# Kernel tuning notes

Hardware: AMD Instinct MI355X
Metric: run time of the kernel (lower is better)

## Reference

```python
import jax, jax.numpy as jnp
import numpy as np

N_NODES = 50000
N_EDGES = 1600000
CHANNELS = 128
EXPANSION = 50
CUTOFF = 5.0
LOG2 = 0.6931471805599453


def shifted_softplus(x):
    return jax.nn.softplus(x) - LOG2


def gaussian_smearing(r, cutoff=CUTOFF, n=EXPANSION):
    # centers evenly spaced in [0, cutoff]; width set by spacing
    centers = jnp.linspace(0.0, cutoff, n, dtype=r.dtype)
    delta = centers[1] - centers[0]
    coef = 1.0 / (2.0 * delta * delta)
    d = r[:, None] - centers[None, :]          # [E, n]
    return jnp.exp(-coef * d * d)


def setup_inputs() -> dict:
    key = jax.random.key(0)
    ks = jax.random.split(key, 12)
    C, F = CHANNELS, EXPANSION

    def lin(k, fan_in, shape):
        bound = 1.0 / np.sqrt(fan_in)
        return jax.random.uniform(k, shape, jnp.float32, -bound, bound)

    return {
        "features": jax.random.normal(ks[0], (N_NODES, C), jnp.float32),
        "edge_distances": jax.random.uniform(ks[1], (N_EDGES,), jnp.float32) * CUTOFF,
        "W_lin": lin(ks[2], C, (C, C)),
        "Wf1": lin(ks[3], F, (F, C)), "bf1": lin(ks[4], F, (C,)),
        "Wf2": lin(ks[5], C, (C, C)), "bf2": lin(ks[6], C, (C,)),
        "Wm1": lin(ks[7], C, (C, C)), "bm1": lin(ks[8], C, (C,)),
        "Wm2": lin(ks[9], C, (C, C)), "bm2": lin(ks[10], C, (C,)),
        "senders": jax.random.randint(ks[11], (N_EDGES,), 0, N_NODES, jnp.int32),
        "receivers": jax.random.randint(jax.random.fold_in(key, 99), (N_EDGES,), 0, N_NODES, jnp.int32),
    }


def reference(features, edge_distances, W_lin, Wf1, bf1, Wf2, bf2,
              Wm1, bm1, Wm2, bm2, senders, receivers):
    # 1. linear transform of node features (no bias)
    h = features @ W_lin.T                                   # [N, C]
    # 2. learnable radial filter F(r_ij): Gaussian basis -> MLP
    basis = gaussian_smearing(edge_distances)                # [E, F]
    ef = shifted_softplus(basis @ Wf1 + bf1) @ Wf2 + bf2     # [E, C]
    # 3. gather neighbour features, elementwise multiply, scatter-sum
    messages = h[senders] * ef                               # [E, C]
    agg = jax.ops.segment_sum(messages, receivers, num_segments=N_NODES)  # [N, C]
    # 4. output MLP
    return shifted_softplus(agg @ Wm1 + bm1) @ Wm2 + bm2
```

## Files before the change

kernel.cpp:

```cpp
#include <hip/hip_runtime.h>
#include <hip/hip_bf16.h>
#include <math.h>

#define N_NODES 50000
#define N_EDGES 1600000
#define CH 128
#define NF 50
#define NR 8192
#define NB 512
#define BUCKET_NODES 98
#define CAP 3584
#define PASSA_CHUNK 4096
#define NBLK_SCAT 391
#define NBLK_TB   128
#define NBLK_DH   782
#define GATHER_NPB 16
#define NBLK_GATH 3125

constexpr float DELTA  = 5.0f / 49.0f;
constexpr float COEF   = 1.0f / (2.0f * DELTA * DELTA);
constexpr float LOG2_  = 0.6931471805599453f;
constexpr float RSCALE = (float)(NR - 1) / 5.0f;

typedef short  bf16x8 __attribute__((ext_vector_type(8)));
typedef float  f32x4  __attribute__((ext_vector_type(4)));
typedef unsigned short ushort_t;
typedef unsigned long long u64;

__device__ __forceinline__ float ssp(float x) {
    return fmaxf(x, 0.0f) + __logf(1.0f + __expf(-fabsf(x))) - LOG2_;
}
__device__ __forceinline__ ushort_t f2bf(float x) {
    __hip_bfloat16 b = __float2bfloat16(x);
    return *reinterpret_cast<ushort_t*>(&b);
}
__device__ __forceinline__ float bf2f(ushort_t u) {
    return __uint_as_float(((unsigned)u) << 16);
}
__device__ __forceinline__ float4 f4zero() { return make_float4(0.f, 0.f, 0.f, 0.f); }

__global__ __launch_bounds__(256) void k1_prep(const float* __restrict__ Wlin,
                                               const float* __restrict__ Wm1,
                                               const float* __restrict__ Wm2,
                                               const float* __restrict__ Wf1,
                                               const float* __restrict__ Wf2,
                                               ushort_t* __restrict__ wlhi,
                                               ushort_t* __restrict__ wllo,
                                               ushort_t* __restrict__ wm1hi,
                                               ushort_t* __restrict__ wm1lo,
                                               ushort_t* __restrict__ wm2hi,
                                               ushort_t* __restrict__ wm2lo,
                                               ushort_t* __restrict__ wf1t,
                                               ushort_t* __restrict__ wf2hi,
                                               ushort_t* __restrict__ wf2lo,
                                               int* __restrict__ bcnt) {
    const int tid = threadIdx.x;
    if (blockIdx.x == 64) {
        bcnt[tid] = 0;
        bcnt[tid + 256] = 0;
        return;
    }
    int idx = blockIdx.x * 256 + tid;
    int n = idx >> 7, k = idx & 127;
    {   float w = Wlin[(size_t)n * CH + k];
        ushort_t hi = f2bf(w); wlhi[n * CH + k] = hi; wllo[n * CH + k] = f2bf(w - bf2f(hi)); }
    {   float w = Wm1[(size_t)k * CH + n];
        ushort_t hi = f2bf(w); wm1hi[n * CH + k] = hi; wm1lo[n * CH + k] = f2bf(w - bf2f(hi)); }
    {   float w = Wm2[(size_t)k * CH + n];
        ushort_t hi = f2bf(w); wm2hi[n * CH + k] = hi; wm2lo[n * CH + k] = f2bf(w - bf2f(hi)); }
    if (k < 64) wf1t[n * 64 + k] = (k < NF) ? f2bf(Wf1[k * CH + n]) : (ushort_t)0;
    {   float w = Wf2[(size_t)k * CH + n];
        ushort_t hi = f2bf(w); wf2hi[n * CH + k] = hi; wf2lo[n * CH + k] = f2bf(w - bf2f(hi)); }
}

__device__ void scatter_body(char* smem, int blk,
                             const int* __restrict__ recv,
                             const int* __restrict__ send,
                             const float* __restrict__ dist,
                             int* __restrict__ bcnt,
                             u64* __restrict__ brec) {
    int* bcur   = (int*)smem;
    int* bbaseL = bcur + NB;
    const int tid = threadIdx.x;
    for (int i = tid; i < NB; i += 256) bcur[i] = 0;
    __syncthreads();
    const int e0 = blk * PASSA_CHUNK;
#pragma unroll
    for (int i = 0; i < 16; i++) {
        int e = e0 + tid + i * 256;
        if (e < N_EDGES) atomicAdd(&bcur[recv[e] / BUCKET_NODES], 1);
    }
    __syncthreads();
    for (int i = tid; i < NB; i += 256) {
        int c = bcur[i];
        bbaseL[i] = c ? atomicAdd(&bcnt[i], c) : 0;
        bcur[i] = 0;
    }
    __syncthreads();
#pragma unroll
    for (int i = 0; i < 16; i++) {
        int e = e0 + tid + i * 256;
        if (e < N_EDGES) {
            int r = recv[e];
            int b = r / BUCKET_NODES;
            int rank = bbaseL[b] + atomicAdd(&bcur[b], 1);
            if (rank < CAP) {
                float x = fminf(dist[e] * RSCALE, (float)(NR - 1));
                int ti = __float2int_rn(x);
                u64 rec = (u64)(unsigned)(send[e] | (r << 16)) | ((u64)ti << 32);
                brec[(size_t)b * CAP + rank] = rec;
            }
        }
    }
}

__device__ void table_body(char* smem, int blk,
                           const float* __restrict__ bf1,
                           const float* __restrict__ bf2,
                           const ushort_t* __restrict__ wf1t,
                           const ushort_t* __restrict__ wf2hi,
                           const ushort_t* __restrict__ wf2lo,
                           ushort_t* __restrict__ tabn) {
    ushort_t (*basis)[72] = (ushort_t (*)[72])smem;
    ushort_t (*t1s)[136]  = (ushort_t (*)[136])(smem + 64 * 72 * 2);
    const int tid = threadIdx.x;
    const int g0  = blk * 64;

    for (int i = tid; i < 64 * 64; i += 256) {
        int e = i >> 6, k = i & 63;
        float val = 0.f;
        if (k < NF) {
            float r = (float)(g0 + e) * (5.0f / (float)(NR - 1));
            float d = r - (float)k * DELTA;
            val = __expf(-COEF * d * d);
        }
        basis[e][k] = f2bf(val);
    }
    __syncthreads();

    const int lane = tid & 63;
    const int wv   = tid >> 6;
    const int row  = lane & 15;
    const int quad = lane >> 4;
    const int c0   = (2 * wv) * 16 + row;
    const int c1   = c0 + 16;

    f32x4 acc[2][4];
#pragma unroll
    for (int j = 0; j < 2; j++)
#pragma unroll
        for (int rt = 0; rt < 4; rt++) acc[j][rt] = (f32x4){0.f, 0.f, 0.f, 0.f};

#pragma unroll
    for (int kb = 0; kb < 64; kb += 32) {
        bf16x8 B0 = *(const bf16x8*)&wf1t[c0 * 64 + kb + quad * 8];
        bf16x8 B1 = *(const bf16x8*)&wf1t[c1 * 64 + kb + quad * 8];
#pragma unroll
        for (int rt = 0; rt < 4; rt++) {
            bf16x8 A = *(const bf16x8*)&basis[rt * 16 + row][kb + quad * 8];
            acc[0][rt] = __builtin_amdgcn_mfma_f32_16x16x32_bf16(A, B0, acc[0][rt], 0, 0, 0);
            acc[1][rt] = __builtin_amdgcn_mfma_f32_16x16x32_bf16(A, B1, acc[1][rt], 0, 0, 0);
        }
    }
    {
        float b1v[2] = { bf1[c0], bf1[c1] };
#pragma unroll
        for (int j = 0; j < 2; j++) {
            int c = j ? c1 : c0;
#pragma unroll
            for (int rt = 0; rt < 4; rt++)
#pragma unroll
                for (int rg = 0; rg < 4; rg++) {
                    int e = rt * 16 + quad * 4 + rg;
                    t1s[e][c] = f2bf(ssp(acc[j][rt][rg] + b1v[j]));
                }
        }
    }
    __syncthreads();

#pragma unroll
    for (int j = 0; j < 2; j++)
#pragma unroll
        for (int rt = 0; rt < 4; rt++) acc[j][rt] = (f32x4){0.f, 0.f, 0.f, 0.f};

#pragma unroll
    for (int kb = 0; kb < 128; kb += 32) {
        bf16x8 B0h = *(const bf16x8*)&wf2hi[c0 * CH + kb + quad * 8];
        bf16x8 B0l = *(const bf16x8*)&wf2lo[c0 * CH + kb + quad * 8];
        bf16x8 B1h = *(const bf16x8*)&wf2hi[c1 * CH + kb + quad * 8];
        bf16x8 B1l = *(const bf16x8*)&wf2lo[c1 * CH + kb + quad * 8];
#pragma unroll
        for (int rt = 0; rt < 4; rt++) {
            bf16x8 A = *(const bf16x8*)&t1s[rt * 16 + row][kb + quad * 8];
            acc[0][rt] = __builtin_amdgcn_mfma_f32_16x16x32_bf16(A, B0l, acc[0][rt], 0, 0, 0);
            acc[0][rt] = __builtin_amdgcn_mfma_f32_16x16x32_bf16(A, B0h, acc[0][rt], 0, 0, 0);
            acc[1][rt] = __builtin_amdgcn_mfma_f32_16x16x32_bf16(A, B1l, acc[1][rt], 0, 0, 0);
            acc[1][rt] = __builtin_amdgcn_mfma_f32_16x16x32_bf16(A, B1h, acc[1][rt], 0, 0, 0);
        }
    }
    {
        float b2v[2] = { bf2[c0], bf2[c1] };
#pragma unroll
        for (int j = 0; j < 2; j++) {
            int c = j ? c1 : c0;
#pragma unroll
            for (int rt = 0; rt < 4; rt++)
#pragma unroll
                for (int rg = 0; rg < 4; rg++) {
                    int g = g0 + rt * 16 + quad * 4 + rg;
                    tabn[(size_t)g * CH + c] = f2bf(acc[j][rt][rg] + b2v[j]);
                }
        }
    }
}

__device__ void dense_h_body(char* smem, int blk,
                             const float* __restrict__ X,
                             const ushort_t* __restrict__ Bhi,
                             const ushort_t* __restrict__ Blo,
                             ushort_t* __restrict__ Y) {
    ushort_t (*xs)[136] = (ushort_t (*)[136])smem;
    const int tid  = threadIdx.x;
    const int row0 = blk * 64;

#pragma unroll
    for (int i = 0; i < 8; i++) {
        int idx = tid + i * 256;
        int r   = idx >> 5;
        int c4  = (idx & 31) * 4;
        float4 v = (row0 + r < N_NODES) ? *(const float4*)&X[(size_t)(row0 + r) * CH + c4]
                                        : f4zero();
        ushort4 s;
        s.x = f2bf(v.x); s.y = f2bf(v.y); s.z = f2bf(v.z); s.w = f2bf(v.w);
        *(ushort4*)&xs[r][c4] = s;
    }
    __syncthreads();

    const int lane = tid & 63;
    const int wv   = tid >> 6;
    const int row  = lane & 15;
    const int quad = lane >> 4;
    const int c0   = (2 * wv) * 16 + row;
    const int c1   = c0 + 16;

    f32x4 acc[2][4];
#pragma unroll
    for (int j = 0; j < 2; j++)
#pragma unroll
        for (int rt = 0; rt < 4; rt++) acc[j][rt] = (f32x4){0.f, 0.f, 0.f, 0.f};

#pragma unroll
    for (int kb = 0; kb < 128; kb += 32) {
        bf16x8 B0h = *(const bf16x8*)&Bhi[(size_t)c0 * CH + kb + quad * 8];
        bf16x8 B0l = *(const bf16x8*)&Blo[(size_t)c0 * CH + kb + quad * 8];
        bf16x8 B1h = *(const bf16x8*)&Bhi[(size_t)c1 * CH + kb + quad * 8];
        bf16x8 B1l = *(const bf16x8*)&Blo[(size_t)c1 * CH + kb + quad * 8];
#pragma unroll
        for (int rt = 0; rt < 4; rt++) {
            bf16x8 A = *(const bf16x8*)&xs[rt * 16 + row][kb + quad * 8];
            acc[0][rt] = __builtin_amdgcn_mfma_f32_16x16x32_bf16(A, B0l, acc[0][rt], 0, 0, 0);
            acc[0][rt] = __builtin_amdgcn_mfma_f32_16x16x32_bf16(A, B0h, acc[0][rt], 0, 0, 0);
            acc[1][rt] = __builtin_amdgcn_mfma_f32_16x16x32_bf16(A, B1l, acc[1][rt], 0, 0, 0);
            acc[1][rt] = __builtin_amdgcn_mfma_f32_16x16x32_bf16(A, B1h, acc[1][rt], 0, 0, 0);
        }
    }

#pragma unroll
    for (int j = 0; j < 2; j++) {
        int c = j ? c1 : c0;
#pragma unroll
        for (int rt = 0; rt < 4; rt++)
#pragma unroll
            for (int rg = 0; rg < 4; rg++) {
                int r = row0 + rt * 16 + quad * 4 + rg;
                if (r < N_NODES) Y[(size_t)r * CH + c] = f2bf(acc[j][rt][rg]);
            }
    }
}

__global__ __launch_bounds__(256) void k2_mega(const int* __restrict__ recv,
                                               const int* __restrict__ send,
                                               const float* __restrict__ dist,
                                               int* __restrict__ bcnt,
                                               u64* __restrict__ brec,
                                               const float* __restrict__ bf1,
                                               const float* __restrict__ bf2,
                                               const ushort_t* __restrict__ wf1t,
                                               const ushort_t* __restrict__ wf2hi,
                                               const ushort_t* __restrict__ wf2lo,
                                               ushort_t* __restrict__ tabn,
                                               const float* __restrict__ X,
                                               const ushort_t* __restrict__ wlhi,
                                               const ushort_t* __restrict__ wllo,
                                               ushort_t* __restrict__ h) {
    __shared__ __align__(16) char smem[64 * 72 * 2 + 64 * 136 * 2];
    const int blk = blockIdx.x;
    if (blk < NBLK_SCAT) {
        scatter_body(smem, blk, recv, send, dist, bcnt, brec);
    } else if (blk < NBLK_SCAT + NBLK_TB) {
        table_body(smem, blk - NBLK_SCAT, bf1, bf2, wf1t, wf2hi, wf2lo, tabn);
    } else {
        dense_h_body(smem, blk - NBLK_SCAT - NBLK_TB, X, wlhi, wllo, h);
    }
}

__global__ __launch_bounds__(256) void bucket_sort(const int* __restrict__ bcnt,
                                                   u64* __restrict__ brec,
                                                   int* __restrict__ nodebeg,
                                                   int* __restrict__ nodecnt) {
    __shared__ int shist[BUCKET_NODES];
    __shared__ int sexc[BUCKET_NODES];
    __shared__ unsigned sout[CAP];
    const int b = blockIdx.x, tid = threadIdx.x;
    const int nbase = b * BUCKET_NODES;
    const int nn = min(BUCKET_NODES, N_NODES - nbase);
    if (nn <= 0) return;
    const int m = min(bcnt[b], CAP);
    const u64* my = brec + (size_t)b * CAP;

    for (int i = tid; i < nn; i += 256) shist[i] = 0;
    __syncthreads();
    for (int i = tid; i < m; i += 256) {
        int l = (int)((my[i] >> 16) & 0xFFFF) - nbase;
        atomicAdd(&shist[l], 1);
    }
    __syncthreads();
    if (tid == 0) {
        int acc = 0;
        for (int l = 0; l < nn; l++) { sexc[l] = acc; acc += shist[l]; }
    }
    __syncthreads();
    for (int l = tid; l < nn; l += 256) {
        nodebeg[nbase + l] = b * (CAP * 2) + sexc[l];
        nodecnt[nbase + l] = shist[l];
    }
    __syncthreads();
    for (int i = tid; i < m; i += 256) {
        u64 rec = my[i];
        int l = (int)((rec >> 16) & 0xFFFF) - nbase;
        int rank = atomicAdd(&sexc[l], 1);
        sout[rank] = (unsigned)(rec & 0xFFFF) | ((unsigned)((rec >> 32) & 0x3FFF) << 16);
    }
    __syncthreads();
    unsigned* out32 = (unsigned*)(brec + (size_t)b * CAP);
    for (int i = tid; i < m; i += 256) out32[i] = sout[i];
}

__global__ __launch_bounds__(256) void gather_nodes(const unsigned* __restrict__ recs,
                                                    const int* __restrict__ nodebeg,
                                                    const int* __restrict__ nodecnt,
                                                    const ushort_t* __restrict__ h,
                                                    const ushort_t* __restrict__ tabn,
                                                    ushort_t* __restrict__ aggb) {
    const int g  = threadIdx.x >> 4;
    const int c8 = (threadIdx.x & 15) * 8;
    const int n  = blockIdx.x * GATHER_NPB + g;
    if (n >= N_NODES) return;
    const int beg = nodebeg[n];
    const int cnt = nodecnt[n];

    float acc[8];
#pragma unroll
    for (int j = 0; j < 8; j++) acc[j] = 0.f;

    int e = 0;
    for (; e + 4 <= cnt; e += 4) {
        unsigned v[4];
#pragma unroll
        for (int u = 0; u < 4; u++) v[u] = recs[beg + e + u];
        bf16x8 hu[4], tn[4];
#pragma unroll
        for (int u = 0; u < 4; u++) {
            int s  = (int)(v[u] & 0xFFFF);
            int ti = (int)(v[u] >> 16);
            hu[u] = *(const bf16x8*)&h[(size_t)s * CH + c8];
            tn[u] = *(const bf16x8*)&tabn[(size_t)ti * CH + c8];
        }
#pragma unroll
        for (int u = 0; u < 4; u++)
#pragma unroll
            for (int j = 0; j < 8; j++)
                acc[j] = fmaf(bf2f((ushort_t)hu[u][j]), bf2f((ushort_t)tn[u][j]), acc[j]);
    }
    for (; e < cnt; e++) {
        unsigned v = recs[beg + e];
        int s  = (int)(v & 0xFFFF);
        int ti = (int)(v >> 16);
        bf16x8 hu = *(const bf16x8*)&h[(size_t)s * CH + c8];
        bf16x8 tn = *(const bf16x8*)&tabn[(size_t)ti * CH + c8];
#pragma unroll
        for (int j = 0; j < 8; j++)
            acc[j] = fmaf(bf2f((ushort_t)hu[j]), bf2f((ushort_t)tn[j]), acc[j]);
    }

    bf16x8 o;
#pragma unroll
    for (int j = 0; j < 8; j++) o[j] = (short)f2bf(acc[j]);
    *(bf16x8*)&aggb[(size_t)n * CH + c8] = o;
}

__global__ __launch_bounds__(256) void out_mlp(const ushort_t* __restrict__ AGG,
                                               const ushort_t* __restrict__ B1hi,
                                               const ushort_t* __restrict__ B1lo,
                                               const float* __restrict__ bm1,
                                               const ushort_t* __restrict__ B2hi,
                                               const ushort_t* __restrict__ B2lo,
                                               const float* __restrict__ bm2,
                                               float* __restrict__ OUT, int M) {
    __shared__ ushort_t xs[64][136];
    __shared__ ushort_t ts[64][136];
    const int tid  = threadIdx.x;
    const int row0 = blockIdx.x * 64;

#pragma unroll
    for (int i = 0; i < 4; i++) {
        int idx = tid + i * 256;
        int r   = idx >> 4;
        int c8  = (idx & 15) * 8;
        uint4 v = (row0 + r < M) ? *(const uint4*)&AGG[(size_t)(row0 + r) * CH + c8]
                                 : make_uint4(0, 0, 0, 0);
        *(uint4*)&xs[r][c8] = v;
    }
    __syncthreads();

    const int lane = tid & 63;
    const int wv   = tid >> 6;
    const int row  = lane & 15;
    const int quad = lane >> 4;
    const int c0   = (2 * wv) * 16 + row;
    const int c1   = c0 + 16;

    f32x4 acc[2][4];
#pragma unroll
    for (int j = 0; j < 2; j++)
#pragma unroll
        for (int rt = 0; rt < 4; rt++) acc[j][rt] = (f32x4){0.f, 0.f, 0.f, 0.f};

#pragma unroll
    for (int kb = 0; kb < 128; kb += 32) {
        bf16x8 B0h = *(const bf16x8*)&B1hi[(size_t)c0 * CH + kb + quad * 8];
        bf16x8 B0l = *(const bf16x8*)&B1lo[(size_t)c0 * CH + kb + quad * 8];
        bf16x8 B1h_ = *(const bf16x8*)&B1hi[(size_t)c1 * CH + kb + quad * 8];
        bf16x8 B1l_ = *(const bf16x8*)&B1lo[(size_t)c1 * CH + kb + quad * 8];
#pragma unroll
        for (int rt = 0; rt < 4; rt++) {
            bf16x8 A = *(const bf16x8*)&xs[rt * 16 + row][kb + quad * 8];
            acc[0][rt] = __builtin_amdgcn_mfma_f32_16x16x32_bf16(A, B0l, acc[0][rt], 0, 0, 0);
            acc[0][rt] = __builtin_amdgcn_mfma_f32_16x16x32_bf16(A, B0h, acc[0][rt], 0, 0, 0);
            acc[1][rt] = __builtin_amdgcn_mfma_f32_16x16x32_bf16(A, B1l_, acc[1][rt], 0, 0, 0);
            acc[1][rt] = __builtin_amdgcn_mfma_f32_16x16x32_bf16(A, B1h_, acc[1][rt], 0, 0, 0);
        }
    }
    {
        float bv[2] = { bm1[c0], bm1[c1] };
#pragma unroll
        for (int j = 0; j < 2; j++) {
            int c = j ? c1 : c0;
#pragma unroll
            for (int rt = 0; rt < 4; rt++)
#pragma unroll
                for (int rg = 0; rg < 4; rg++)
                    ts[rt * 16 + quad * 4 + rg][c] = f2bf(ssp(acc[j][rt][rg] + bv[j]));
        }
    }
    __syncthreads();

#pragma unroll
    for (int j = 0; j < 2; j++)
#pragma unroll
        for (int rt = 0; rt < 4; rt++) acc[j][rt] = (f32x4){0.f, 0.f, 0.f, 0.f};

#pragma unroll
    for (int kb = 0; kb < 128; kb += 32) {
        bf16x8 B0h = *(const bf16x8*)&B2hi[(size_t)c0 * CH + kb + quad * 8];
        bf16x8 B0l = *(const bf16x8*)&B2lo[(size_t)c0 * CH + kb + quad * 8];
        bf16x8 B1h_ = *(const bf16x8*)&B2hi[(size_t)c1 * CH + kb + quad * 8];
        bf16x8 B1l_ = *(const bf16x8*)&B2lo[(size_t)c1 * CH + kb + quad * 8];
#pragma unroll
        for (int rt = 0; rt < 4; rt++) {
            bf16x8 A = *(const bf16x8*)&ts[rt * 16 + row][kb + quad * 8];
            acc[0][rt] = __builtin_amdgcn_mfma_f32_16x16x32_bf16(A, B0l, acc[0][rt], 0, 0, 0);
            acc[0][rt] = __builtin_amdgcn_mfma_f32_16x16x32_bf16(A, B0h, acc[0][rt], 0, 0, 0);
            acc[1][rt] = __builtin_amdgcn_mfma_f32_16x16x32_bf16(A, B1l_, acc[1][rt], 0, 0, 0);
            acc[1][rt] = __builtin_amdgcn_mfma_f32_16x16x32_bf16(A, B1h_, acc[1][rt], 0, 0, 0);
        }
    }
    {
        float bv[2] = { bm2[c0], bm2[c1] };
#pragma unroll
        for (int j = 0; j < 2; j++) {
            int c = j ? c1 : c0;
#pragma unroll
            for (int rt = 0; rt < 4; rt++)
#pragma unroll
                for (int rg = 0; rg < 4; rg++) {
                    int r = row0 + rt * 16 + quad * 4 + rg;
                    if (r < M) OUT[(size_t)r * CH + c] = acc[j][rt][rg] + bv[j];
                }
        }
    }
}

extern "C" void kernel_launch(void* const* d_in, const int* in_sizes, int n_in,
                              void* d_out, int out_size, void* d_ws, size_t ws_size,
                              hipStream_t stream) {
    const float* features = (const float*)d_in[0];
    const float* dist     = (const float*)d_in[1];
    const float* W_lin    = (const float*)d_in[2];
    const float* Wf1      = (const float*)d_in[3];
    const float* bf1      = (const float*)d_in[4];
    const float* Wf2      = (const float*)d_in[5];
    const float* bf2      = (const float*)d_in[6];
    const float* Wm1      = (const float*)d_in[7];
    const float* bm1      = (const float*)d_in[8];
    const float* Wm2      = (const float*)d_in[9];
    const float* bm2      = (const float*)d_in[10];
    const int* senders    = (const int*)d_in[11];
    const int* receivers  = (const int*)d_in[12];
    float* out = (float*)d_out;

    u64* brec       = (u64*)d_ws;
    ushort_t* h     = (ushort_t*)(brec + (size_t)NB * CAP);
    ushort_t* aggb  = h + (size_t)N_NODES * CH;
    ushort_t* tabn  = aggb + (size_t)N_NODES * CH;
    int* bcnt       = (int*)(tabn + (size_t)NR * CH);
    ushort_t* wlhi  = (ushort_t*)(bcnt + NB);
    ushort_t* wllo  = wlhi  + CH * CH;
    ushort_t* wm1hi = wllo  + CH * CH;
    ushort_t* wm1lo = wm1hi + CH * CH;
    ushort_t* wm2hi = wm1lo + CH * CH;
    ushort_t* wm2lo = wm2hi + CH * CH;
    ushort_t* wf1t  = wm2lo + CH * CH;
    ushort_t* wf2hi = wf1t  + CH * 64;
    ushort_t* wf2lo = wf2hi + CH * CH;
    int* nodebeg    = (int*)(wf2lo + CH * CH);
    int* nodecnt    = nodebeg + N_NODES;

    k1_prep<<<65, 256, 0, stream>>>(W_lin, Wm1, Wm2, Wf1, Wf2,
                                    wlhi, wllo, wm1hi, wm1lo, wm2hi, wm2lo,
                                    wf1t, wf2hi, wf2lo, bcnt);

    k2_mega<<<NBLK_SCAT + NBLK_TB + NBLK_DH, 256, 0, stream>>>(
        receivers, senders, dist, bcnt, brec,
        bf1, bf2, wf1t, wf2hi, wf2lo, tabn,
        features, wlhi, wllo, h);

    bucket_sort<<<NB, 256, 0, stream>>>(bcnt, brec, nodebeg, nodecnt);

    gather_nodes<<<NBLK_GATH, 256, 0, stream>>>((const unsigned*)brec,
                                                nodebeg, nodecnt, h, tabn, aggb);

    out_mlp<<<NBLK_DH, 256, 0, stream>>>(aggb, wm1hi, wm1lo, bm1,
                                         wm2hi, wm2lo, bm2, out, N_NODES);
}
```

Measured before the change: 270.5 us.

## Fuse bucket sort with neighbour gather and shrink buckets to 25 nodes

The separate bucket_sort and gather_nodes kernels are merged into one sort_gather kernel. Each block sorts its bucket's edge records into shared memory and then immediately accumulates the h·filter products for its nodes from those records. This removes the global write-back and re-read of the sorted records and the nodebeg/nodecnt arrays, and drops one kernel launch. Buckets are made smaller (2048 buckets, 25 nodes, capacity 1024), the gather loop is unrolled by 8, and nontemporal loads and stores are added. The cost is that each block walks its nodes with 16 groups in two uneven rounds, and the per-bucket capacity margin is tighter.

```diff
diff --git a/kernel.cpp b/kernel.cpp
--- a/kernel.cpp
+++ b/kernel.cpp
@@ -7,15 +7,13 @@
 #define CH 128
 #define NF 50
 #define NR 8192
-#define NB 512
-#define BUCKET_NODES 98
-#define CAP 3584
+#define NB 2048
+#define BUCKET_NODES 25
+#define CAP 1024
 #define PASSA_CHUNK 4096
 #define NBLK_SCAT 391
 #define NBLK_TB   128
 #define NBLK_DH   782
-#define GATHER_NPB 16
-#define NBLK_GATH 3125
 
 constexpr float DELTA  = 5.0f / 49.0f;
 constexpr float COEF   = 1.0f / (2.0f * DELTA * DELTA);
@@ -56,8 +54,7 @@
                                                int* __restrict__ bcnt) {
     const int tid = threadIdx.x;
     if (blockIdx.x == 64) {
-        bcnt[tid] = 0;
-        bcnt[tid + 256] = 0;
+        for (int i = tid; i < NB; i += 256) bcnt[i] = 0;
         return;
     }
     int idx = blockIdx.x * 256 + tid;
@@ -108,7 +105,7 @@
                 float x = fminf(dist[e] * RSCALE, (float)(NR - 1));
                 int ti = __float2int_rn(x);
                 u64 rec = (u64)(unsigned)(send[e] | (r << 16)) | ((u64)ti << 32);
-                brec[(size_t)b * CAP + rank] = rec;
+                __builtin_nontemporal_store(rec, &brec[(size_t)b * CAP + rank]);
             }
         }
     }
@@ -304,11 +301,13 @@
     }
 }
 
-__global__ __launch_bounds__(256) void bucket_sort(const int* __restrict__ bcnt,
-                                                   u64* __restrict__ brec,
-                                                   int* __restrict__ nodebeg,
-                                                   int* __restrict__ nodecnt) {
+__global__ __launch_bounds__(256) void sort_gather(const int* __restrict__ bcnt,
+                                                   const u64* __restrict__ brec,
+                                                   const ushort_t* __restrict__ h,
+                                                   const ushort_t* __restrict__ tabn,
+                                                   ushort_t* __restrict__ aggb) {
     __shared__ int shist[BUCKET_NODES];
+    __shared__ int sbeg[BUCKET_NODES];
     __shared__ int sexc[BUCKET_NODES];
     __shared__ unsigned sout[CAP];
     const int b = blockIdx.x, tid = threadIdx.x;
@@ -321,82 +320,88 @@
     for (int i = tid; i < nn; i += 256) shist[i] = 0;
     __syncthreads();
     for (int i = tid; i < m; i += 256) {
-        int l = (int)((my[i] >> 16) & 0xFFFF) - nbase;
+        u64 rec = __builtin_nontemporal_load(&my[i]);
+        int l = (int)((rec >> 16) & 0xFFFF) - nbase;
         atomicAdd(&shist[l], 1);
     }
     __syncthreads();
     if (tid == 0) {
         int acc = 0;
-        for (int l = 0; l < nn; l++) { sexc[l] = acc; acc += shist[l]; }
-    }
-    __syncthreads();
-    for (int l = tid; l < nn; l += 256) {
-        nodebeg[nbase + l] = b * (CAP * 2) + sexc[l];
-        nodecnt[nbase + l] = shist[l];
+#pragma unroll
+        for (int l = 0; l < BUCKET_NODES; l++) {
+            if (l < nn) { sexc[l] = acc; sbeg[l] = acc; acc += shist[l]; }
+        }
     }
     __syncthreads();
     for (int i = tid; i < m; i += 256) {
-        u64 rec = my[i];
+        u64 rec = __builtin_nontemporal_load(&my[i]);
         int l = (int)((rec >> 16) & 0xFFFF) - nbase;
         int rank = atomicAdd(&sexc[l], 1);
         sout[rank] = (unsigned)(rec & 0xFFFF) | ((unsigned)((rec >> 32) & 0x3FFF) << 16);
     }
     __syncthreads();
-    unsigned* out32 = (unsigned*)(brec + (size_t)b * CAP);
-    for (int i = tid; i < m; i += 256) out32[i] = sout[i];
-}
-
-__global__ __launch_bounds__(256) void gather_nodes(const unsigned* __restrict__ recs,
-                                                    const int* __restrict__ nodebeg,
-                                                    const int* __restrict__ nodecnt,
-                                                    const ushort_t* __restrict__ h,
-                                                    const ushort_t* __restrict__ tabn,
-                                                    ushort_t* __restrict__ aggb) {
-    const int g  = threadIdx.x >> 4;
-    const int c8 = (threadIdx.x & 15) * 8;
-    const int n  = blockIdx.x * GATHER_NPB + g;
-    if (n >= N_NODES) return;
-    const int beg = nodebeg[n];
-    const int cnt = nodecnt[n];
-
-    float acc[8];
-#pragma unroll
-    for (int j = 0; j < 8; j++) acc[j] = 0.f;
-
-    int e = 0;
-    for (; e + 4 <= cnt; e += 4) {
-        unsigned v[4];
-#pragma unroll
-        for (int u = 0; u < 4; u++) v[u] = recs[beg + e + u];
-        bf16x8 hu[4], tn[4];
-#pragma unroll
-        for (int u = 0; u < 4; u++) {
-            int s  = (int)(v[u] & 0xFFFF);
-            int ti = (int)(v[u] >> 16);
-            hu[u] = *(const bf16x8*)&h[(size_t)s * CH + c8];
-            tn[u] = *(const bf16x8*)&tabn[(size_t)ti * CH + c8];
-        }
-#pragma unroll
-        for (int u = 0; u < 4; u++)
+
+    const int g  = tid >> 4;
+    const int c8 = (tid & 15) * 8;
+    for (int l = g; l < nn; l += 16) {
+        const int beg = sbeg[l], end = sbeg[l] + shist[l];
+        float acc[8];
+#pragma unroll
+        for (int j = 0; j < 8; j++) acc[j] = 0.f;
+
+        int e = beg;
+        for (; e + 8 <= end; e += 8) {
+            unsigned v[8];
+#pragma unroll
+            for (int u = 0; u < 8; u++) v[u] = sout[e + u];
+            bf16x8 hu[8], tn[8];
+#pragma unroll
+            for (int u = 0; u < 8; u++) {
+                int s  = (int)(v[u] & 0xFFFF);
+                int ti = (int)(v[u] >> 16);
+                hu[u] = *(const bf16x8*)&h[(size_t)s * CH + c8];
+                tn[u] = *(const bf16x8*)&tabn[(size_t)ti * CH + c8];
+            }
+#pragma unroll
+            for (int u = 0; u < 8; u++)
+#pragma unroll
+                for (int j = 0; j < 8; j++)
+                    acc[j] = fmaf(bf2f((ushort_t)hu[u][j]), bf2f((ushort_t)tn[u][j]), acc[j]);
+        }
+        for (; e + 4 <= end; e += 4) {
+            unsigned v[4];
+#pragma unroll
+            for (int u = 0; u < 4; u++) v[u] = sout[e + u];
+            bf16x8 hu[4], tn[4];
+#pragma unroll
+            for (int u = 0; u < 4; u++) {
+                int s  = (int)(v[u] & 0xFFFF);
+                int ti = (int)(v[u] >> 16);
+                hu[u] = *(const bf16x8*)&h[(size_t)s * CH + c8];
+                tn[u] = *(const bf16x8*)&tabn[(size_t)ti * CH + c8];
+            }
+#pragma unroll
+            for (int u = 0; u < 4; u++)
+#pragma unroll
+                for (int j = 0; j < 8; j++)
+                    acc[j] = fmaf(bf2f((ushort_t)hu[u][j]), bf2f((ushort_t)tn[u][j]), acc[j]);
+        }
+        for (; e < end; e++) {
+            unsigned v = sout[e];
+            int s  = (int)(v & 0xFFFF);
+            int ti = (int)(v >> 16);
+            bf16x8 hu = *(const bf16x8*)&h[(size_t)s * CH + c8];
+            bf16x8 tn = *(const bf16x8*)&tabn[(size_t)ti * CH + c8];
 #pragma unroll
             for (int j = 0; j < 8; j++)
-                acc[j] = fmaf(bf2f((ushort_t)hu[u][j]), bf2f((ushort_t)tn[u][j]), acc[j]);
-    }
-    for (; e < cnt; e++) {
-        unsigned v = recs[beg + e];
-        int s  = (int)(v & 0xFFFF);
-        int ti = (int)(v >> 16);
-        bf16x8 hu = *(const bf16x8*)&h[(size_t)s * CH + c8];
-        bf16x8 tn = *(const bf16x8*)&tabn[(size_t)ti * CH + c8];
-#pragma unroll
-        for (int j = 0; j < 8; j++)
-            acc[j] = fmaf(bf2f((ushort_t)hu[j]), bf2f((ushort_t)tn[j]), acc[j]);
-    }
-
-    bf16x8 o;
-#pragma unroll
-    for (int j = 0; j < 8; j++) o[j] = (short)f2bf(acc[j]);
-    *(bf16x8*)&aggb[(size_t)n * CH + c8] = o;
+                acc[j] = fmaf(bf2f((ushort_t)hu[j]), bf2f((ushort_t)tn[j]), acc[j]);
+        }
+
+        bf16x8 o;
+#pragma unroll
+        for (int j = 0; j < 8; j++) o[j] = (short)f2bf(acc[j]);
+        __builtin_nontemporal_store(o, (bf16x8*)&aggb[(size_t)(nbase + l) * CH + c8]);
+    }
 }
 
 __global__ __launch_bounds__(256) void out_mlp(const ushort_t* __restrict__ AGG,
@@ -533,8 +538,6 @@
     ushort_t* wf1t  = wm2lo + CH * CH;
     ushort_t* wf2hi = wf1t  + CH * 64;
     ushort_t* wf2lo = wf2hi + CH * CH;
-    int* nodebeg    = (int*)(wf2lo + CH * CH);
-    int* nodecnt    = nodebeg + N_NODES;
 
     k1_prep<<<65, 256, 0, stream>>>(W_lin, Wm1, Wm2, Wf1, Wf2,
                                     wlhi, wllo, wm1hi, wm1lo, wm2hi, wm2lo,
@@ -545,10 +548,7 @@
         bf1, bf2, wf1t, wf2hi, wf2lo, tabn,
         features, wlhi, wllo, h);
 
-    bucket_sort<<<NB, 256, 0, stream>>>(bcnt, brec, nodebeg, nodecnt);
-
-    gather_nodes<<<NBLK_GATH, 256, 0, stream>>>((const unsigned*)brec,
-                                                nodebeg, nodecnt, h, tabn, aggb);
+    sort_gather<<<NB, 256, 0, stream>>>(bcnt, brec, h, tabn, aggb);
 
     out_mlp<<<NBLK_DH, 256, 0, stream>>>(aggb, wm1hi, wm1lo, bm1,
                                          wm2hi, wm2lo, bm2, out, N_NODES);
```

New measurement: 268.5 us. No clear change (-0.7%).
